# Performance work log

Hardware: AMD Instinct MI355X
Metric: run time of the kernel (lower is better)

The kernel has to match this reference:

```python
import jax, jax.numpy as jnp
import numpy as np

B, S, D, H, DH, L, MLP, VOCAB = 1, 2048, 512, 8, 64, 6, 2048, 256
BLOCK, C = 128, 32
EPS = 1e-6
NEG = -1e9


def layer_norm(x, scale, bias):
    mu = jnp.mean(x, axis=-1, keepdims=True)
    var = jnp.mean(jnp.square(x - mu), axis=-1, keepdims=True)
    return (x - mu) * jax.lax.rsqrt(var + EPS) * scale + bias


def sparse_pattern_mask(seq_len):
    # Union of Fixed1 (same causal block) and Fixed2 (last c columns of each
    # block), both intersected with the causal mask. Shape [S, S] bool.
    i = jnp.arange(seq_len)[:, None]
    j = jnp.arange(seq_len)[None, :]
    causal = j <= i
    fixed1 = (i // BLOCK) == (j // BLOCK)
    fixed2 = (j % BLOCK) >= (BLOCK - C)
    return causal & (fixed1 | fixed2)


def setup_inputs() -> dict:
    key = jax.random.key(0)
    ks = jax.random.split(key, 12)
    s = 0.02
    inp = {
        'tokens': jax.random.randint(ks[0], (B, S), 0, VOCAB, dtype=jnp.int32),
        'embed': jax.random.normal(ks[1], (VOCAB, D), jnp.float32) * s,
        'pos_emb': jax.random.normal(ks[2], (1, S, D), jnp.float32) * s,
        'ln1_scale': jnp.ones((L, D), jnp.float32),
        'ln1_bias': jnp.zeros((L, D), jnp.float32),
        'wq': jax.random.normal(ks[3], (L, D, H, DH), jnp.float32) * s,
        'wk': jax.random.normal(ks[4], (L, D, H, DH), jnp.float32) * s,
        'wv': jax.random.normal(ks[5], (L, D, H, DH), jnp.float32) * s,
        'wo': jax.random.normal(ks[6], (L, H, DH, D), jnp.float32) * s,
        'ln2_scale': jnp.ones((L, D), jnp.float32),
        'ln2_bias': jnp.zeros((L, D), jnp.float32),
        'w1': jax.random.normal(ks[7], (L, D, MLP), jnp.float32) * s,
        'b1': jnp.zeros((L, MLP), jnp.float32),
        'w2': jax.random.normal(ks[8], (L, MLP, D), jnp.float32) * s,
        'b2': jnp.zeros((L, D), jnp.float32),
        'lnf_scale': jnp.ones((D,), jnp.float32),
        'lnf_bias': jnp.zeros((D,), jnp.float32),
        'wout': jax.random.normal(ks[9], (D, VOCAB), jnp.float32) * s,
        'bout': jnp.zeros((VOCAB,), jnp.float32),
    }
    return inp


def _forward(tokens, embed, pos_emb, ln1_scale, ln1_bias, wq, wk, wv, wo,
             ln2_scale, ln2_bias, w1, b1, w2, b2, lnf_scale, lnf_bias,
             wout, bout):
    # padding mask computed on unshifted inputs (keys with token==0 are masked)
    key_pad = tokens > 0                               # [B, S]
    # shift right (decoder teacher forcing)
    shifted = jnp.pad(tokens, ((0, 0), (1, 0)))[:, :-1]
    x = embed[shifted] + pos_emb                       # [B, S, D]

    pattern = sparse_pattern_mask(S)                   # [S, S]
    mask = pattern[None, None] & key_pad[:, None, None, :]  # [B,1,S,S]

    for l in range(L):
        h = layer_norm(x, ln1_scale[l], ln1_bias[l])
        q = jnp.einsum('bsd,dhk->bshk', h, wq[l]) / jnp.sqrt(
            jnp.asarray(DH, x.dtype))
        k = jnp.einsum('bsd,dhk->bshk', h, wk[l])
        v = jnp.einsum('bsd,dhk->bshk', h, wv[l])
        scores = jnp.einsum('bqhk,bshk->bhqs', q, k)   # [B,H,S,S]
        scores = jnp.where(mask, scores, NEG)
        probs = jax.nn.softmax(scores, axis=-1)
        o = jnp.einsum('bhqs,bshk->bqhk', probs, v)
        x = x + jnp.einsum('bqhk,hkd->bqd', o, wo[l])

        y = layer_norm(x, ln2_scale[l], ln2_bias[l])
        y = jax.nn.gelu(y @ w1[l] + b1[l])
        x = x + (y @ w2[l] + b2[l])

    x = layer_norm(x, lnf_scale, lnf_bias)
    return x @ wout + bout                             # [B, S, VOCAB]


def reference(tokens, embed, pos_emb, ln1_scale, ln1_bias, wq, wk, wv, wo,
              ln2_scale, ln2_bias, w1, b1, w2, b2, lnf_scale, lnf_bias,
              wout, bout):
    return _forward(tokens, embed, pos_emb, ln1_scale, ln1_bias, wq, wk, wv,
                    wo, ln2_scale, ln2_bias, w1, b1, w2, b2, lnf_scale,
                    lnf_bias, wout, bout)
```

## Files before the change

kernel.cpp:

```cpp
#include <hip/hip_runtime.h>
#include <hip/hip_bf16.h>
#include <cstdint>
#include <cstddef>

#define DEV __device__ __forceinline__

namespace {

constexpr int S    = 2048;
constexpr int D    = 512;
constexpr int H    = 8;
constexpr int DH   = 64;
constexpr int NL   = 6;
constexpr int MLPD = 2048;
constexpr int VOC  = 256;
constexpr int QS   = 1536;
constexpr float EPSF = 1e-6f;

typedef unsigned short u16;
typedef __attribute__((ext_vector_type(8))) short s8v;
typedef __attribute__((ext_vector_type(4))) float f4v;

DEV float u2f(u16 u){
  union { unsigned int i; float f; } t; t.i = ((unsigned int)u) << 16; return t.f;
}
DEV short bfr(float f){
  __hip_bfloat16 h = __float2bfloat16(f);
  short s; __builtin_memcpy(&s, &h, 2); return s;
}
DEV float gelu_fast(float x){
  float z = 0.7978845608028654f * (x + 0.044715f * x * x * x);
  return x / (1.f + __expf(-2.f * z));
}
DEV void gll16(const u16* gp, u16* lp){
  __builtin_amdgcn_global_load_lds(
      (const __attribute__((address_space(1))) unsigned int*)gp,
      (__attribute__((address_space(3))) unsigned int*)lp, 16, 0, 0);
}

__global__ void k_embed(const int* __restrict__ tokens, const float* __restrict__ emb,
                        const float* __restrict__ pos, float* __restrict__ x){
  int s = blockIdx.x;
  int tok = (s == 0) ? 0 : tokens[s - 1];
  if (tok < 0) tok = 0; if (tok >= VOC) tok = VOC - 1;
  const float* er = emb + (size_t)tok * D;
  const float* pr = pos + (size_t)s * D;
  float* xr = x + (size_t)s * D;
  for (int d = threadIdx.x; d < D; d += blockDim.x)
    xr[d] = er[d] + pr[d];
}

template<int HASP>
__global__ __launch_bounds__(256)
void k_lnr(const float* __restrict__ P0, const float* __restrict__ P1,
           const float* __restrict__ bias, float* __restrict__ x,
           const float* __restrict__ sc, const float* __restrict__ bi,
           u16* __restrict__ out)
{
  int s = blockIdx.x * 4 + (threadIdx.x >> 6), t = threadIdx.x & 63;
  size_t base = (size_t)s * D;
  float v[8]; float sum = 0.f, sq = 0.f;
  #pragma unroll
  for (int e = 0; e < 8; ++e){
    int d = t + 64 * e;
    size_t idx = base + d;
    float xv = x[idx];
    if (HASP){
      float bv = bias ? bias[d] : 0.f;
      xv += P0[idx] + P1[idx] + bv;
      x[idx] = xv;
    }
    v[e] = xv; sum += xv; sq += xv * xv;
  }
  #pragma unroll
  for (int off = 32; off >= 1; off >>= 1){
    sum += __shfl_down(sum, off, 64);
    sq  += __shfl_down(sq,  off, 64);
  }
  sum = __shfl(sum, 0, 64); sq = __shfl(sq, 0, 64);
  float mu  = sum * (1.f / (float)D);
  float var = sq * (1.f / (float)D) - mu * mu;
  float r = rsqrtf(var + EPSF);
  u16* orow = out + base;
  #pragma unroll
  for (int e = 0; e < 8; ++e){
    int d = t + 64 * e;
    orow[d] = (u16)bfr((v[e] - mu) * r * sc[d] + bi[d]);
  }
}

__global__ __launch_bounds__(256)
void k_wt(const float* __restrict__ src, u16* __restrict__ dst, int R, int C,
          size_t sStr, size_t dStr){
  src += (size_t)blockIdx.z * sStr;
  dst += (size_t)blockIdx.z * dStr;
  __shared__ float tb[32][33];
  int c0 = blockIdx.x * 32, r0 = blockIdx.y * 32;
  int tc = threadIdx.x & 31, tr8 = threadIdx.x >> 5;
  #pragma unroll
  for (int rr = 0; rr < 32; rr += 8)
    tb[rr + tr8][tc] = src[(size_t)(r0 + rr + tr8) * C + c0 + tc];
  __syncthreads();
  #pragma unroll
  for (int rr = 0; rr < 32; rr += 8)
    dst[(size_t)(c0 + rr + tr8) * R + r0 + tc] = (u16)bfr(tb[tc][rr + tr8]);
}

__global__ __launch_bounds__(256)
void k_wt4(const float* __restrict__ wq, const float* __restrict__ wk,
           const float* __restrict__ wv, const float* __restrict__ wo,
           u16* __restrict__ wqkvT, u16* __restrict__ woT)
{
  const size_t L512 = (size_t)512 * 512;
  int fam = blockIdx.z / 6, l = blockIdx.z % 6;
  const float* src;
  u16* dst;
  if (fam == 0){ src = wq + (size_t)l * L512; dst = wqkvT + (size_t)l * QS * 512; }
  else if (fam == 1){ src = wk + (size_t)l * L512; dst = wqkvT + (size_t)l * QS * 512 + 512 * 512; }
  else if (fam == 2){ src = wv + (size_t)l * L512; dst = wqkvT + (size_t)l * QS * 512 + 1024 * 512; }
  else { src = wo + (size_t)l * L512; dst = woT + (size_t)l * L512; }
  __shared__ float tb[32][33];
  int c0 = blockIdx.x * 32, r0 = blockIdx.y * 32;
  int tc = threadIdx.x & 31, tr8 = threadIdx.x >> 5;
  #pragma unroll
  for (int rr = 0; rr < 32; rr += 8)
    tb[rr + tr8][tc] = src[(size_t)(r0 + rr + tr8) * 512 + c0 + tc];
  __syncthreads();
  #pragma unroll
  for (int rr = 0; rr < 32; rr += 8)
    dst[(size_t)(c0 + rr + tr8) * 512 + r0 + tc] = (u16)bfr(tb[tc][rr + tr8]);
}

template<int FM, int FN, int MODE>
__global__ __launch_bounds__(64)
void k_gd(const u16* __restrict__ A, const u16* __restrict__ Bt,
          const float* __restrict__ bias, float* __restrict__ Cf,
          u16* __restrict__ Cb, int N, int K, float alpha)
{
  const int nx = gridDim.x;
  const int nwg = nx * gridDim.y;
  int wg = blockIdx.y * nx + blockIdx.x;
  wg = (wg & 7) * (nwg >> 3) + (wg >> 3);
  const int m0 = (wg / nx) * (FM * 16), n0 = (wg % nx) * (FN * 16);
  const int lane = threadIdx.x, lr = lane & 15, lg = lane >> 4;
  const u16* ap = A  + (size_t)(m0 + lr) * K + lg * 8;
  const u16* bp = Bt + (size_t)(n0 + lr) * K + lg * 8;
  f4v acc[FM][FN] = {};
  #pragma unroll 4
  for (int k0 = 0; k0 < K; k0 += 32){
    s8v af[FM], bf[FN];
    #pragma unroll
    for (int fi = 0; fi < FM; ++fi)
      af[fi] = *reinterpret_cast<const s8v*>(ap + (size_t)fi * 16 * K + k0);
    #pragma unroll
    for (int fj = 0; fj < FN; ++fj)
      bf[fj] = *reinterpret_cast<const s8v*>(bp + (size_t)fj * 16 * K + k0);
    #pragma unroll
    for (int fi = 0; fi < FM; ++fi)
      #pragma unroll
      for (int fj = 0; fj < FN; ++fj)
        acc[fi][fj] = __builtin_amdgcn_mfma_f32_16x16x32_bf16(af[fi], bf[fj], acc[fi][fj], 0, 0, 0);
  }
  #pragma unroll
  for (int fi = 0; fi < FM; ++fi)
    #pragma unroll
    for (int fj = 0; fj < FN; ++fj)
      #pragma unroll
      for (int r = 0; r < 4; ++r){
        int row = m0 + fi * 16 + lg * 4 + r;
        int col = n0 + fj * 16 + lr;
        size_t idx = (size_t)row * N + col;
        float v = acc[fi][fj][r];
        if (MODE == 1)      Cb[idx] = (u16)bfr(gelu_fast(v + bias[col]));
        else if (MODE == 2) Cf[idx] += v + (bias ? bias[col] : 0.f);
        else if (MODE == 3) Cf[idx] = v + bias[col];
        else {
          float al = (col < 512) ? alpha : 1.f;
          Cb[idx] = (u16)bfr(v * al);
        }
      }
}

template<int MODE>
__global__ __launch_bounds__(256)
void k_gs(const u16* __restrict__ A, const u16* __restrict__ Bt,
          const float* __restrict__ bias, u16* __restrict__ Cb,
          int N, int K)
{
  __shared__ __align__(16) u16 As[128 * 32];
  __shared__ __align__(16) u16 Bs[64 * 32];
  const int nx = gridDim.x;
  const int nwg = nx * gridDim.y;
  int wg = blockIdx.y * nx + blockIdx.x;
  wg = (wg & 7) * (nwg >> 3) + (wg >> 3);
  const int m0 = (wg / nx) * 128, n0 = (wg % nx) * 64;
  const int w = threadIdx.x >> 6, lane = threadIdx.x & 63;
  const int lr = lane & 15, lg = lane >> 4;
  const int wr = w >> 1, wc = w & 1;
  const int srow = lane >> 2, scd = lane & 3;
  const int swA0 = ((srow) ^ (srow >> 2)) & 3;
  f4v acc[4][2] = {};
  for (int k0 = 0; k0 < K; k0 += 32){
    __syncthreads();
    #pragma unroll
    for (int j = w; j < 8; j += 4){
      int row = j * 16 + srow;
      int g = scd ^ swA0;
      gll16(A + (size_t)(m0 + row) * K + k0 + g * 8, As + j * 512);
    }
    {
      int row = w * 16 + srow;
      int g = scd ^ swA0;
      gll16(Bt + (size_t)(n0 + row) * K + k0 + g * 8, Bs + w * 512);
    }
    asm volatile("s_waitcnt vmcnt(0)" ::: "memory");
    __syncthreads();
    s8v af[4], bf[2];
    #pragma unroll
    for (int fi = 0; fi < 4; ++fi){
      int row = wr * 64 + fi * 16 + lr;
      int slot = lg ^ ((row ^ (row >> 2)) & 3);
      af[fi] = *reinterpret_cast<const s8v*>(As + row * 32 + slot * 8);
    }
    #pragma unroll
    for (int fj = 0; fj < 2; ++fj){
      int row = wc * 32 + fj * 16 + lr;
      int slot = lg ^ ((row ^ (row >> 2)) & 3);
      bf[fj] = *reinterpret_cast<const s8v*>(Bs + row * 32 + slot * 8);
    }
    #pragma unroll
    for (int fi = 0; fi < 4; ++fi)
      #pragma unroll
      for (int fj = 0; fj < 2; ++fj)
        acc[fi][fj] = __builtin_amdgcn_mfma_f32_16x16x32_bf16(af[fi], bf[fj], acc[fi][fj], 0, 0, 0);
  }
  #pragma unroll
  for (int fi = 0; fi < 4; ++fi)
    #pragma unroll
    for (int fj = 0; fj < 2; ++fj)
      #pragma unroll
      for (int r = 0; r < 4; ++r){
        int row = m0 + wr * 64 + fi * 16 + lg * 4 + r;
        int col = n0 + wc * 32 + fj * 16 + lr;
        float v = acc[fi][fj][r];
        if (MODE == 1) Cb[(size_t)row * N + col] = (u16)bfr(gelu_fast(v + bias[col]));
      }
}

template<int MODE>
__global__ __launch_bounds__(256)
void k_gi(const u16* __restrict__ A, const u16* __restrict__ Bt,
          const float* __restrict__ bias, u16* __restrict__ vt,
          u16* __restrict__ Cb, int N, int K, float alpha)
{
  __shared__ float Ls[2][64][65];
  const int nx = gridDim.x;
  const int nwg = nx * gridDim.y;
  int wg = blockIdx.y * nx + blockIdx.x;
  wg = (wg & 7) * (nwg >> 3) + (wg >> 3);
  const int m0 = (wg / nx) * 64, n0 = (wg % nx) * 64;
  const int w = threadIdx.x >> 6, lane = threadIdx.x & 63;
  const int lr = lane & 15, lg = lane >> 4;
  const int KC = K >> 2;
  const u16* ap = A  + (size_t)(m0 + lr) * K + w * KC + lg * 8;
  const u16* bp = Bt + (size_t)(n0 + lr) * K + w * KC + lg * 8;
  f4v acc[4][4] = {};
  #pragma unroll 4
  for (int k0 = 0; k0 < KC; k0 += 32){
    s8v af[4], bf[4];
    #pragma unroll
    for (int fi = 0; fi < 4; ++fi)
      af[fi] = *reinterpret_cast<const s8v*>(ap + (size_t)fi * 16 * K + k0);
    #pragma unroll
    for (int fj = 0; fj < 4; ++fj)
      bf[fj] = *reinterpret_cast<const s8v*>(bp + (size_t)fj * 16 * K + k0);
    #pragma unroll
    for (int fi = 0; fi < 4; ++fi)
      #pragma unroll
      for (int fj = 0; fj < 4; ++fj)
        acc[fi][fj] = __builtin_amdgcn_mfma_f32_16x16x32_bf16(af[fi], bf[fj], acc[fi][fj], 0, 0, 0);
  }
  if (w >= 2){
    #pragma unroll
    for (int fi = 0; fi < 4; ++fi)
      #pragma unroll
      for (int fj = 0; fj < 4; ++fj)
        #pragma unroll
        for (int r = 0; r < 4; ++r)
          Ls[w - 2][lane][fi * 16 + fj * 4 + r] = acc[fi][fj][r];
  }
  __syncthreads();
  if (w < 2){
    #pragma unroll
    for (int fi = 0; fi < 4; ++fi)
      #pragma unroll
      for (int fj = 0; fj < 4; ++fj)
        #pragma unroll
        for (int r = 0; r < 4; ++r)
          acc[fi][fj][r] += Ls[w][lane][fi * 16 + fj * 4 + r];
    if (w == 1){
      #pragma unroll
      for (int fi = 0; fi < 4; ++fi)
        #pragma unroll
        for (int fj = 0; fj < 4; ++fj)
          #pragma unroll
          for (int r = 0; r < 4; ++r)
            Ls[1][lane][fi * 16 + fj * 4 + r] = acc[fi][fj][r];
    }
  }
  __syncthreads();
  if (w == 0){
    #pragma unroll
    for (int fi = 0; fi < 4; ++fi)
      #pragma unroll
      for (int fj = 0; fj < 4; ++fj)
        #pragma unroll
        for (int r = 0; r < 4; ++r){
          acc[fi][fj][r] += Ls[1][lane][fi * 16 + fj * 4 + r];
          Ls[0][lane][fi * 16 + fj * 4 + r] = acc[fi][fj][r];
        }
  }
  __syncthreads();
  #pragma unroll
  for (int fj = 0; fj < 4; ++fj)
    #pragma unroll
    for (int r = 0; r < 4; ++r){
      float v = Ls[0][lane][w * 16 + fj * 4 + r];
      int row = m0 + w * 16 + lg * 4 + r;
      int col = n0 + fj * 16 + lr;
      if (MODE == 1){
        Cb[(size_t)row * N + col] = (u16)bfr(gelu_fast(v + bias[col]));
      } else {
        if (col < 512){
          Cb[(size_t)row * N + col] = (u16)bfr(v * alpha);
        } else if (col < 1024){
          Cb[(size_t)row * N + col] = (u16)bfr(v);
        } else {
          vt[(size_t)(col - 1024) * S + row] = (u16)bfr(v);
        }
      }
    }
}

template<int FM, int FN>
__global__ __launch_bounds__(64)
void k_gds(const u16* __restrict__ A, const u16* __restrict__ Bt,
           float* __restrict__ P, int N, int K, int KC)
{
  const int nx = gridDim.x;
  const int nwg = nx * gridDim.y;
  const int M = gridDim.y * (FM * 16);
  int wg = blockIdx.y * nx + blockIdx.x;
  wg = (wg & 7) * (nwg >> 3) + (wg >> 3);
  const int m0 = (wg / nx) * (FM * 16), n0 = (wg % nx) * (FN * 16);
  const int z = blockIdx.z;
  const int lane = threadIdx.x, lr = lane & 15, lg = lane >> 4;
  const u16* ap = A  + (size_t)(m0 + lr) * K + z * KC + lg * 8;
  const u16* bp = Bt + (size_t)(n0 + lr) * K + z * KC + lg * 8;
  P += (size_t)z * M * N;
  f4v acc[FM][FN] = {};
  #pragma unroll 4
  for (int k0 = 0; k0 < KC; k0 += 32){
    s8v af[FM], bf[FN];
    #pragma unroll
    for (int fi = 0; fi < FM; ++fi)
      af[fi] = *reinterpret_cast<const s8v*>(ap + (size_t)fi * 16 * K + k0);
    #pragma unroll
    for (int fj = 0; fj < FN; ++fj)
      bf[fj] = *reinterpret_cast<const s8v*>(bp + (size_t)fj * 16 * K + k0);
    #pragma unroll
    for (int fi = 0; fi < FM; ++fi)
      #pragma unroll
      for (int fj = 0; fj < FN; ++fj)
        acc[fi][fj] = __builtin_amdgcn_mfma_f32_16x16x32_bf16(af[fi], bf[fj], acc[fi][fj], 0, 0, 0);
  }
  #pragma unroll
  for (int fi = 0; fi < FM; ++fi)
    #pragma unroll
    for (int fj = 0; fj < FN; ++fj)
      #pragma unroll
      for (int r = 0; r < 4; ++r){
        int row = m0 + fi * 16 + lg * 4 + r;
        int col = n0 + fj * 16 + lr;
        P[(size_t)row * N + col] = acc[fi][fj][r];
      }
}

__global__ __launch_bounds__(64)
void k_mattn(const u16* __restrict__ qp_, const u16* __restrict__ kp_,
             const u16* __restrict__ vt, const int* __restrict__ tokens,
             u16* __restrict__ ob)
{
  const int q0 = (gridDim.x - 1 - blockIdx.x) * 16;
  const int h  = blockIdx.y;
  const int B  = q0 >> 7;
  const int lane = threadIdx.x, lr = lane & 15, lg = lane >> 4;

  __shared__ __align__(16) u16 Ps[16][40];

  const u16* qrow = qp_ + (size_t)(q0 + lr) * QS + h * DH;
  s8v qf0 = *reinterpret_cast<const s8v*>(qrow + lg * 8);
  s8v qf1 = *reinterpret_cast<const s8v*>(qrow + 32 + lg * 8);

  f4v o0 = {}, o1 = {}, o2 = {}, o3 = {};
  float m[4] = {-1e30f, -1e30f, -1e30f, -1e30f};
  float l[4] = {0.f, 0.f, 0.f, 0.f};

  const int ntiles = B + ((q0 & 127) >> 5) + 1;

  for (int tt = 0; tt < ntiles; ++tt){
    int kbase; bool causal;
    if (tt < B){ kbase = tt * 128 + 96; causal = false; }
    else       { kbase = B * 128 + (tt - B) * 32; causal = (kbase + 31 > q0); }

    f4v s0 = {}, s1 = {};
    const u16* k0p = kp_ + (size_t)(kbase + lr) * QS + h * DH;
    const u16* k1p = kp_ + (size_t)(kbase + 16 + lr) * QS + h * DH;
    s8v kf;
    kf = *reinterpret_cast<const s8v*>(k0p + lg * 8);
    s0 = __builtin_amdgcn_mfma_f32_16x16x32_bf16(qf0, kf, s0, 0, 0, 0);
    kf = *reinterpret_cast<const s8v*>(k0p + 32 + lg * 8);
    s0 = __builtin_amdgcn_mfma_f32_16x16x32_bf16(qf1, kf, s0, 0, 0, 0);
    kf = *reinterpret_cast<const s8v*>(k1p + lg * 8);
    s1 = __builtin_amdgcn_mfma_f32_16x16x32_bf16(qf0, kf, s1, 0, 0, 0);
    kf = *reinterpret_cast<const s8v*>(k1p + 32 + lg * 8);
    s1 = __builtin_amdgcn_mfma_f32_16x16x32_bf16(qf1, kf, s1, 0, 0, 0);

    const int tok0 = tokens[kbase + lr] > 0;
    const int tok1 = tokens[kbase + 16 + lr] > 0;
    #pragma unroll
    for (int r = 0; r < 4; ++r){
      int qg = q0 + 4 * lg + r;
      float a0 = (tok0 && (!causal || kbase + lr <= qg))      ? s0[r] : -1e30f;
      float a1 = (tok1 && (!causal || kbase + 16 + lr <= qg)) ? s1[r] : -1e30f;
      float tm = fmaxf(a0, a1);
      tm = fmaxf(tm, __shfl_xor(tm, 1, 64));
      tm = fmaxf(tm, __shfl_xor(tm, 2, 64));
      tm = fmaxf(tm, __shfl_xor(tm, 4, 64));
      tm = fmaxf(tm, __shfl_xor(tm, 8, 64));
      float mn = fmaxf(m[r], tm);
      bool dead = (mn <= -1e29f);
      float sc = dead ? 1.f : __expf(m[r] - mn);
      float p0 = dead ? 0.f : __expf(a0 - mn);
      float p1 = dead ? 0.f : __expf(a1 - mn);
      l[r] = l[r] * sc + p0 + p1;
      m[r] = mn;
      o0[r] *= sc; o1[r] *= sc; o2[r] *= sc; o3[r] *= sc;
      Ps[4 * lg + r][lr]      = (u16)bfr(p0);
      Ps[4 * lg + r][16 + lr] = (u16)bfr(p1);
    }

    asm volatile("s_waitcnt lgkmcnt(0)" ::: "memory");
    __builtin_amdgcn_sched_barrier(0);
    s8v pf  = *reinterpret_cast<const s8v*>(&Ps[lr][lg * 8]);
    const u16* vtb = vt + (size_t)(h * DH + lr) * S + kbase + lg * 8;
    s8v vf0 = *reinterpret_cast<const s8v*>(vtb);
    s8v vf1 = *reinterpret_cast<const s8v*>(vtb + (size_t)16 * S);
    s8v vf2 = *reinterpret_cast<const s8v*>(vtb + (size_t)32 * S);
    s8v vf3 = *reinterpret_cast<const s8v*>(vtb + (size_t)48 * S);
    o0 = __builtin_amdgcn_mfma_f32_16x16x32_bf16(pf, vf0, o0, 0, 0, 0);
    o1 = __builtin_amdgcn_mfma_f32_16x16x32_bf16(pf, vf1, o1, 0, 0, 0);
    o2 = __builtin_amdgcn_mfma_f32_16x16x32_bf16(pf, vf2, o2, 0, 0, 0);
    o3 = __builtin_amdgcn_mfma_f32_16x16x32_bf16(pf, vf3, o3, 0, 0, 0);
  }

  #pragma unroll
  for (int r = 0; r < 4; ++r){
    float lt = l[r];
    lt += __shfl_xor(lt, 1, 64);
    lt += __shfl_xor(lt, 2, 64);
    lt += __shfl_xor(lt, 4, 64);
    lt += __shfl_xor(lt, 8, 64);
    int qg = q0 + 4 * lg + r;
    u16* orow = ob + (size_t)qg * D + h * DH;
    if (lt <= 0.f){
      #pragma unroll
      for (int c4 = 0; c4 < 4; ++c4){
        const u16* vr = vt + (size_t)(h * DH + c4 * 16 + lr) * S;
        float s = 0.f;
        for (int j = 0; j < S; ++j) s += u2f(vr[j]);
        orow[c4 * 16 + lr] = (u16)bfr(s * (1.f / (float)S));
      }
    } else {
      float inv = 1.f / lt;
      orow[lr]      = (u16)bfr(o0[r] * inv);
      orow[16 + lr] = (u16)bfr(o1[r] * inv);
      orow[32 + lr] = (u16)bfr(o2[r] * inv);
      orow[48 + lr] = (u16)bfr(o3[r] * inv);
    }
  }
}

}

extern "C" void kernel_launch(void* const* d_in, const int* in_sizes, int n_in,
                              void* d_out, int out_size, void* d_ws, size_t ws_size,
                              hipStream_t stream)
{
  (void)n_in; (void)out_size; (void)ws_size;

  int I_tok=0, I_emb=1, I_pos=2, I_l1s=3, I_l1b=4, I_wq=5, I_wk=6, I_wv=7,
      I_wo=8, I_l2s=9, I_l2b=10, I_w1=11, I_b1=12, I_w2=13, I_b2=14,
      I_lfs=15, I_lfb=16, I_wout=17, I_bout=18;
  if (in_sizes[0] != S){
    I_b1=0;  I_b2=1;  I_bout=2; I_emb=3;  I_l1b=4; I_l1s=5;  I_l2b=6;
    I_l2s=7; I_lfb=8; I_lfs=9;  I_pos=10; I_tok=11; I_w1=12; I_w2=13;
    I_wk=14; I_wo=15; I_wout=16; I_wq=17; I_wv=18;
  }

  const int*   tokens = (const int*)d_in[I_tok];
  const float* emb  = (const float*)d_in[I_emb];
  const float* pos  = (const float*)d_in[I_pos];
  const float* ln1s = (const float*)d_in[I_l1s];
  const float* ln1b = (const float*)d_in[I_l1b];
  const float* wq   = (const float*)d_in[I_wq];
  const float* wk   = (const float*)d_in[I_wk];
  const float* wv   = (const float*)d_in[I_wv];
  const float* wo   = (const float*)d_in[I_wo];
  const float* ln2s = (const float*)d_in[I_l2s];
  const float* ln2b = (const float*)d_in[I_l2b];
  const float* w1   = (const float*)d_in[I_w1];
  const float* b1   = (const float*)d_in[I_b1];
  const float* w2   = (const float*)d_in[I_w2];
  const float* b2   = (const float*)d_in[I_b2];
  const float* lnfs = (const float*)d_in[I_lfs];
  const float* lnfb = (const float*)d_in[I_lfb];
  const float* wout = (const float*)d_in[I_wout];
  const float* bout = (const float*)d_in[I_bout];
  float* outp = (float*)d_out;

  char* ws = (char*)d_ws;
  float* x    = (float*)(ws);
  u16*  hb    = (u16*)(ws + ((size_t)4  << 20));
  u16*  qkvb  = (u16*)(ws + ((size_t)6  << 20));
  u16*  ob    = (u16*)(ws + ((size_t)12 << 20));
  u16*  gb    = (u16*)(ws + ((size_t)14 << 20));
  u16*  vtb   = (u16*)(ws + ((size_t)14 << 20));
  float* pWO  = (float*)(ws + ((size_t)14 << 20));
  float* pW2  = (float*)(ws + ((size_t)6  << 20));
  u16*  wqkvT = (u16*)(ws + ((size_t)23 << 20));
  u16*  w1T   = (u16*)(ws + ((size_t)32 << 20));
  u16*  w2T   = (u16*)(ws + ((size_t)44 << 20));
  u16*  woT   = (u16*)(ws + ((size_t)56 << 20));
  u16*  woutT = (u16*)(ws + ((size_t)59 << 20));

  const size_t L512 = (size_t)512 * 512;
  const size_t LMLP = (size_t)512 * 2048;
  const size_t SM   = (size_t)S * 512;

  k_wt4<<<dim3(16, 16, 24), dim3(256), 0, stream>>>(wq, wk, wv, wo, wqkvT, woT);
  k_wt<<<dim3(64, 16, 6), dim3(256), 0, stream>>>(w1, w1T, 512, 2048, LMLP, LMLP);
  k_wt<<<dim3(16, 64, 6), dim3(256), 0, stream>>>(w2, w2T, 2048, 512, LMLP, LMLP);
  k_wt<<<dim3(8,  16, 1), dim3(256), 0, stream>>>(wout, woutT, 512, 256, 0, 0);

  k_embed<<<dim3(S), dim3(128), 0, stream>>>(tokens, emb, pos, x);

  for (int l = 0; l < NL; ++l){
    if (l == 0){
      k_lnr<0><<<dim3(S/4), dim3(256), 0, stream>>>(
          nullptr, nullptr, nullptr, x, ln1s, ln1b, hb);
    }
    k_gi<4><<<dim3(24, 32), dim3(256), 0, stream>>>(
        hb, wqkvT + (size_t)l * QS * 512, nullptr, vtb, qkvb, QS, 512, 0.125f);
    k_mattn<<<dim3(S/16, H), dim3(64), 0, stream>>>(
        qkvb, qkvb + 512, vtb, tokens, ob);
    k_gds<2,4><<<dim3(8, 64, 2), dim3(64), 0, stream>>>(
        ob, woT + (size_t)l * L512, pWO, 512, 512, 256);
    k_lnr<1><<<dim3(S/4), dim3(256), 0, stream>>>(
        pWO, pWO + SM, nullptr, x, ln2s + (size_t)l*D, ln2b + (size_t)l*D, hb);
    k_gs<1><<<dim3(32, 16), dim3(256), 0, stream>>>(
        hb, w1T + (size_t)l * LMLP, b1 + (size_t)l*MLPD, gb, MLPD, 512);
    k_gds<2,4><<<dim3(8, 64, 2), dim3(64), 0, stream>>>(
        gb, w2T + (size_t)l * LMLP, pW2, 512, 2048, 1024);
    if (l < NL - 1){
      k_lnr<1><<<dim3(S/4), dim3(256), 0, stream>>>(
          pW2, pW2 + SM, b2 + (size_t)l*D, x,
          ln1s + (size_t)(l+1)*D, ln1b + (size_t)(l+1)*D, hb);
    } else {
      k_lnr<1><<<dim3(S/4), dim3(256), 0, stream>>>(
          pW2, pW2 + SM, b2 + (size_t)l*D, x, lnfs, lnfb, hb);
    }
  }

  k_gd<2,4,3><<<dim3(4, 64), dim3(64), 0, stream>>>(
      hb, woutT, bout, outp, nullptr, VOC, 512, 1.f);
}
```

Before: 718.0 us.

## Replace split-K QKV GEMM with LDS-staged 128x64 tiled kernel

The QKV projection kernel drops its intra-block split-K design, where four waves each reduced a K quarter directly from global memory and then summed partials through shared memory. It now stages 128x32 A and 64x32 B tiles into swizzled LDS with direct global-to-LDS loads, and each wave computes a 64x32 output sub-tile over the full K. This removes the cross-wave reduction and its barriers and reuses loaded tiles across waves. In exchange it halves the grid to 384 blocks and adds a barrier per K step with no double buffering, so load latency is not overlapped.

```diff
diff --git a/kernel.cpp b/kernel.cpp
--- a/kernel.cpp
+++ b/kernel.cpp
@@ -247,90 +247,67 @@
       }
 }
 
-template<int MODE>
 __global__ __launch_bounds__(256)
-void k_gi(const u16* __restrict__ A, const u16* __restrict__ Bt,
-          const float* __restrict__ bias, u16* __restrict__ vt,
-          u16* __restrict__ Cb, int N, int K, float alpha)
-{
-  __shared__ float Ls[2][64][65];
+void k_gsq(const u16* __restrict__ A, const u16* __restrict__ Bt,
+           u16* __restrict__ vt, u16* __restrict__ Cb, float alpha)
+{
+  constexpr int K = 512, N = QS;
+  __shared__ __align__(16) u16 As[128 * 32];
+  __shared__ __align__(16) u16 Bs[64 * 32];
   const int nx = gridDim.x;
   const int nwg = nx * gridDim.y;
   int wg = blockIdx.y * nx + blockIdx.x;
   wg = (wg & 7) * (nwg >> 3) + (wg >> 3);
-  const int m0 = (wg / nx) * 64, n0 = (wg % nx) * 64;
+  const int m0 = (wg / nx) * 128, n0 = (wg % nx) * 64;
   const int w = threadIdx.x >> 6, lane = threadIdx.x & 63;
   const int lr = lane & 15, lg = lane >> 4;
-  const int KC = K >> 2;
-  const u16* ap = A  + (size_t)(m0 + lr) * K + w * KC + lg * 8;
-  const u16* bp = Bt + (size_t)(n0 + lr) * K + w * KC + lg * 8;
-  f4v acc[4][4] = {};
-  #pragma unroll 4
-  for (int k0 = 0; k0 < KC; k0 += 32){
-    s8v af[4], bf[4];
+  const int wr = w >> 1, wc = w & 1;
+  const int srow = lane >> 2, scd = lane & 3;
+  const int swA0 = ((srow) ^ (srow >> 2)) & 3;
+  f4v acc[4][2] = {};
+  for (int k0 = 0; k0 < K; k0 += 32){
+    __syncthreads();
+    #pragma unroll
+    for (int j = w; j < 8; j += 4){
+      int row = j * 16 + srow;
+      int g = scd ^ swA0;
+      gll16(A + (size_t)(m0 + row) * K + k0 + g * 8, As + j * 512);
+    }
+    {
+      int row = w * 16 + srow;
+      int g = scd ^ swA0;
+      gll16(Bt + (size_t)(n0 + row) * K + k0 + g * 8, Bs + w * 512);
+    }
+    asm volatile("s_waitcnt vmcnt(0)" ::: "memory");
+    __syncthreads();
+    s8v af[4], bf[2];
+    #pragma unroll
+    for (int fi = 0; fi < 4; ++fi){
+      int row = wr * 64 + fi * 16 + lr;
+      int slot = lg ^ ((row ^ (row >> 2)) & 3);
+      af[fi] = *reinterpret_cast<const s8v*>(As + row * 32 + slot * 8);
+    }
+    #pragma unroll
+    for (int fj = 0; fj < 2; ++fj){
+      int row = wc * 32 + fj * 16 + lr;
+      int slot = lg ^ ((row ^ (row >> 2)) & 3);
+      bf[fj] = *reinterpret_cast<const s8v*>(Bs + row * 32 + slot * 8);
+    }
     #pragma unroll
     for (int fi = 0; fi < 4; ++fi)
-      af[fi] = *reinterpret_cast<const s8v*>(ap + (size_t)fi * 16 * K + k0);
-    #pragma unroll
-    for (int fj = 0; fj < 4; ++fj)
-      bf[fj] = *reinterpret_cast<const s8v*>(bp + (size_t)fj * 16 * K + k0);
-    #pragma unroll
-    for (int fi = 0; fi < 4; ++fi)
-      #pragma unroll
-      for (int fj = 0; fj < 4; ++fj)
+      #pragma unroll
+      for (int fj = 0; fj < 2; ++fj)
         acc[fi][fj] = __builtin_amdgcn_mfma_f32_16x16x32_bf16(af[fi], bf[fj], acc[fi][fj], 0, 0, 0);
   }
-  if (w >= 2){
-    #pragma unroll
-    for (int fi = 0; fi < 4; ++fi)
-      #pragma unroll
-      for (int fj = 0; fj < 4; ++fj)
-        #pragma unroll
-        for (int r = 0; r < 4; ++r)
-          Ls[w - 2][lane][fi * 16 + fj * 4 + r] = acc[fi][fj][r];
-  }
-  __syncthreads();
-  if (w < 2){
-    #pragma unroll
-    for (int fi = 0; fi < 4; ++fi)
-      #pragma unroll
-      for (int fj = 0; fj < 4; ++fj)
-        #pragma unroll
-        for (int r = 0; r < 4; ++r)
-          acc[fi][fj][r] += Ls[w][lane][fi * 16 + fj * 4 + r];
-    if (w == 1){
-      #pragma unroll
-      for (int fi = 0; fi < 4; ++fi)
-        #pragma unroll
-        for (int fj = 0; fj < 4; ++fj)
-          #pragma unroll
-          for (int r = 0; r < 4; ++r)
-            Ls[1][lane][fi * 16 + fj * 4 + r] = acc[fi][fj][r];
-    }
-  }
-  __syncthreads();
-  if (w == 0){
-    #pragma unroll
-    for (int fi = 0; fi < 4; ++fi)
-      #pragma unroll
-      for (int fj = 0; fj < 4; ++fj)
-        #pragma unroll
-        for (int r = 0; r < 4; ++r){
-          acc[fi][fj][r] += Ls[1][lane][fi * 16 + fj * 4 + r];
-          Ls[0][lane][fi * 16 + fj * 4 + r] = acc[fi][fj][r];
-        }
-  }
-  __syncthreads();
-  #pragma unroll
-  for (int fj = 0; fj < 4; ++fj)
-    #pragma unroll
-    for (int r = 0; r < 4; ++r){
-      float v = Ls[0][lane][w * 16 + fj * 4 + r];
-      int row = m0 + w * 16 + lg * 4 + r;
-      int col = n0 + fj * 16 + lr;
-      if (MODE == 1){
-        Cb[(size_t)row * N + col] = (u16)bfr(gelu_fast(v + bias[col]));
-      } else {
+  #pragma unroll
+  for (int fi = 0; fi < 4; ++fi)
+    #pragma unroll
+    for (int fj = 0; fj < 2; ++fj)
+      #pragma unroll
+      for (int r = 0; r < 4; ++r){
+        int row = m0 + wr * 64 + fi * 16 + lg * 4 + r;
+        int col = n0 + wc * 32 + fj * 16 + lr;
+        float v = acc[fi][fj][r];
         if (col < 512){
           Cb[(size_t)row * N + col] = (u16)bfr(v * alpha);
         } else if (col < 1024){
@@ -339,7 +316,6 @@
           vt[(size_t)(col - 1024) * S + row] = (u16)bfr(v);
         }
       }
-    }
 }
 
 template<int FM, int FN>
@@ -560,8 +536,8 @@
       k_lnr<0><<<dim3(S/4), dim3(256), 0, stream>>>(
           nullptr, nullptr, nullptr, x, ln1s, ln1b, hb);
     }
-    k_gi<4><<<dim3(24, 32), dim3(256), 0, stream>>>(
-        hb, wqkvT + (size_t)l * QS * 512, nullptr, vtb, qkvb, QS, 512, 0.125f);
+    k_gsq<<<dim3(24, 16), dim3(256), 0, stream>>>(
+        hb, wqkvT + (size_t)l * QS * 512, vtb, qkvb, 0.125f);
     k_mattn<<<dim3(S/16, H), dim3(64), 0, stream>>>(
         qkvb, qkvb + 512, vtb, tokens, ob);
     k_gds<2,4><<<dim3(8, 64, 2), dim3(64), 0, stream>>>(
```

Result: faster. 689.6 us (-4.0%).
